# Performance work log

Hardware: AMD Instinct MI355X
Metric: run time of the kernel (lower is better)

## Reference

```python
import jax, jax.numpy as jnp
import numpy as np

B, L, E = 256, 500, 300  # bsz, max_doc_len, word_embed_dim
KS = [3, 5, 7]           # filters_size


def setup_inputs() -> dict:
    key = jax.random.key(0)
    ks = jax.random.split(key, 1 + 2 * len(KS))
    inp = {"x": jax.random.normal(ks[0], (B, L, E), jnp.float32)}
    i = 1
    for k in KS:
        # PyTorch Conv2d default init scale ~ 1/sqrt(fan_in)
        inp[f"aw{k}"] = jax.random.normal(ks[i], (k, E), jnp.float32) / np.sqrt(k * E).astype(np.float32); i += 1
        inp[f"ab{k}"] = jnp.zeros((1,), jnp.float32)
        inp[f"cw{k}"] = jax.random.normal(ks[i], (E,), jnp.float32) / np.sqrt(E).astype(np.float32); i += 1
        inp[f"cb{k}"] = jnpp = jnp.zeros((1,), jnp.float32)
    return inp


def _branch(x, aw, ab, cw, cb):
    # x: (B, L, E); aw: (k, E); cw: (E,)
    k = aw.shape[0]
    p = (k - 1) // 2
    x4 = x[:, None, :, :]            # NCHW: (B, 1, L, E)
    w4 = aw[None, None, :, :]        # OIHW: (1, 1, k, E)
    s = jax.lax.conv_general_dilated(x4, w4, window_strides=(1, 1),
                                     padding=((p, p), (0, 0)))  # (B, 1, L, 1)
    score = jax.nn.sigmoid(s + ab[0])[:, 0, :, :]               # (B, L, 1)
    gated = x * score                                           # broadcast over E
    # Conv2d(1,1,(1,E)) == per-timestep dot product over E
    return jnp.tanh(jnp.einsum('ble,e->bl', gated, cw) + cb[0])  # (B, L)


def reference(x, aw3, ab3, cw3, cb3, aw5, ab5, cw5, cb5, aw7, ab7, cw7, cb7):
    return (_branch(x, aw3, ab3, cw3, cb3),
            _branch(x, aw5, ab5, cw5, cb5),
            _branch(x, aw7, ab7, cw7, cb7))
```

## Files before the change

kernel.cpp:

```cpp
#include <hip/hip_runtime.h>
#include <math.h>

#define BB 256
#define LL 500
#define EE 300
#define NROWS (BB * LL)
#define NJ 18
#define TOUT 56
#define NTILE 9
#define DROWS 64

__global__ __launch_bounds__(256) void fused_kernel(
    const float* __restrict__ x,
    const float* __restrict__ aw3, const float* __restrict__ ab3,
    const float* __restrict__ cw3, const float* __restrict__ cb3,
    const float* __restrict__ aw5, const float* __restrict__ ab5,
    const float* __restrict__ cw5, const float* __restrict__ cb5,
    const float* __restrict__ aw7, const float* __restrict__ ab7,
    const float* __restrict__ cw7, const float* __restrict__ cb7,
    float* __restrict__ out)
{
    __shared__ float dlds[DROWS][NJ + 1];

    const int b    = blockIdx.x / NTILE;
    const int t    = blockIdx.x % NTILE;
    const int l0   = t * TOUT - 3;
    const int wave = threadIdx.x >> 6;
    const int lane = threadIdx.x & 63;
    const int g    = lane >> 4;
    const int j    = lane & 15;
    const int lr   = wave * 16 + g * 4;

    bool valid[4];
    const float4* xr[4];
#pragma unroll
    for (int rr = 0; rr < 4; ++rr) {
        const int l = l0 + lr + rr;
        valid[rr] = (l >= 0) && (l < LL);
        const int lc = l < 0 ? 0 : (l >= LL ? LL - 1 : l);
        xr[rr] = (const float4*)(x + ((size_t)b * LL + lc) * EE);
    }

    const float* const wptr[NJ] = {
        aw3, aw3 + 300, aw3 + 600, cw3,
        aw5, aw5 + 300, aw5 + 600, aw5 + 900, aw5 + 1200, cw5,
        aw7, aw7 + 300, aw7 + 600, aw7 + 900, aw7 + 1200, aw7 + 1500, aw7 + 1800, cw7
    };

    float acc[NJ][4];
#pragma unroll
    for (int d = 0; d < NJ; ++d)
#pragma unroll
        for (int rr = 0; rr < 4; ++rr) acc[d][rr] = 0.0f;

#define BODY(c)                                                                     \
    {                                                                               \
        const float4 x0 = xr[0][(c)];                                               \
        const float4 x1 = xr[1][(c)];                                               \
        const float4 x2 = xr[2][(c)];                                               \
        const float4 x3 = xr[3][(c)];                                               \
        _Pragma("unroll")                                                           \
        for (int d = 0; d < NJ; ++d) {                                              \
            const float4 w = ((const float4*)wptr[d])[(c)];                         \
            acc[d][0] = fmaf(x0.w, w.w, fmaf(x0.z, w.z, fmaf(x0.y, w.y, fmaf(x0.x, w.x, acc[d][0])))); \
            acc[d][1] = fmaf(x1.w, w.w, fmaf(x1.z, w.z, fmaf(x1.y, w.y, fmaf(x1.x, w.x, acc[d][1])))); \
            acc[d][2] = fmaf(x2.w, w.w, fmaf(x2.z, w.z, fmaf(x2.y, w.y, fmaf(x2.x, w.x, acc[d][2])))); \
            acc[d][3] = fmaf(x3.w, w.w, fmaf(x3.z, w.z, fmaf(x3.y, w.y, fmaf(x3.x, w.x, acc[d][3])))); \
        }                                                                           \
    }

    BODY(j)
    BODY(j + 16)
    BODY(j + 32)
    BODY(j + 48)
    if (j < 11) {
        BODY(j + 64)
    }
#undef BODY

#pragma unroll
    for (int d = 0; d < NJ; ++d)
#pragma unroll
        for (int rr = 0; rr < 4; ++rr) {
            float v = acc[d][rr];
            v += __shfl_xor(v, 1, 16);
            v += __shfl_xor(v, 2, 16);
            v += __shfl_xor(v, 4, 16);
            v += __shfl_xor(v, 8, 16);
            acc[d][rr] = v;
        }

#pragma unroll
    for (int rr = 0; rr < 4; ++rr) {
        if (j == rr) {
            const float vf = valid[rr] ? 1.0f : 0.0f;
#pragma unroll
            for (int d = 0; d < NJ; ++d) dlds[lr + rr][d] = acc[d][rr] * vf;
        }
    }

    __syncthreads();

    const int tid = threadIdx.x;
    if (tid < TOUT) {
        const int lo = t * TOUT + tid;
        if (lo < LL) {
            const int c = tid + 3;

            float pre3 = 0.0f, pre5 = 0.0f, pre7 = 0.0f;
#pragma unroll
            for (int tp = 0; tp < 3; ++tp) pre3 += dlds[c + tp - 1][tp];
#pragma unroll
            for (int tp = 0; tp < 5; ++tp) pre5 += dlds[c + tp - 2][4 + tp];
#pragma unroll
            for (int tp = 0; tp < 7; ++tp) pre7 += dlds[c + tp - 3][10 + tp];

            const float c3v = dlds[c][3];
            const float c5v = dlds[c][9];
            const float c7v = dlds[c][17];

            const float s3 = 1.0f / (1.0f + expf(-(pre3 + ab3[0])));
            const float s5 = 1.0f / (1.0f + expf(-(pre5 + ab5[0])));
            const float s7 = 1.0f / (1.0f + expf(-(pre7 + ab7[0])));

            const int r = b * LL + lo;
            out[r]             = tanhf(s3 * c3v + cb3[0]);
            out[NROWS + r]     = tanhf(s5 * c5v + cb5[0]);
            out[2 * NROWS + r] = tanhf(s7 * c7v + cb7[0]);
        }
    }
}

extern "C" void kernel_launch(void* const* d_in, const int* in_sizes, int n_in,
                              void* d_out, int out_size, void* d_ws, size_t ws_size,
                              hipStream_t stream) {
    const float* x   = (const float*)d_in[0];
    const float* aw3 = (const float*)d_in[1];
    const float* ab3 = (const float*)d_in[2];
    const float* cw3 = (const float*)d_in[3];
    const float* cb3 = (const float*)d_in[4];
    const float* aw5 = (const float*)d_in[5];
    const float* ab5 = (const float*)d_in[6];
    const float* cw5 = (const float*)d_in[7];
    const float* cb5 = (const float*)d_in[8];
    const float* aw7 = (const float*)d_in[9];
    const float* ab7 = (const float*)d_in[10];
    const float* cw7 = (const float*)d_in[11];
    const float* cb7 = (const float*)d_in[12];

    float* out = (float*)d_out;

    fused_kernel<<<BB * NTILE, 256, 0, stream>>>(
        x, aw3, ab3, cw3, cb3, aw5, ab5, cw5, cb5, aw7, ab7, cw7, cb7, out);
}
```

Before: 266.4 us.

## Stage filter weights in LDS and software-prefetch x rows

```diff
diff --git a/kernel.cpp b/kernel.cpp
--- a/kernel.cpp
+++ b/kernel.cpp
@@ -6,11 +6,12 @@
 #define EE 300
 #define NROWS (BB * LL)
 #define NJ 18
+#define NC 75
 #define TOUT 56
 #define NTILE 9
 #define DROWS 64
 
-__global__ __launch_bounds__(256) void fused_kernel(
+__global__ __launch_bounds__(256, 4) void fused_kernel(
     const float* __restrict__ x,
     const float* __restrict__ aw3, const float* __restrict__ ab3,
     const float* __restrict__ cw3, const float* __restrict__ cb3,
@@ -20,13 +21,38 @@
     const float* __restrict__ cw7, const float* __restrict__ cb7,
     float* __restrict__ out)
 {
+    __shared__ float4 wlds[NJ][NC];
     __shared__ float dlds[DROWS][NJ + 1];
+    __shared__ const float4* wbase[NJ];
+
+    const int tid = threadIdx.x;
+
+    if (tid == 0) {
+        wbase[0]  = (const float4*)(aw3);
+        wbase[1]  = (const float4*)(aw3 + 300);
+        wbase[2]  = (const float4*)(aw3 + 600);
+        wbase[3]  = (const float4*)(cw3);
+        wbase[4]  = (const float4*)(aw5);
+        wbase[5]  = (const float4*)(aw5 + 300);
+        wbase[6]  = (const float4*)(aw5 + 600);
+        wbase[7]  = (const float4*)(aw5 + 900);
+        wbase[8]  = (const float4*)(aw5 + 1200);
+        wbase[9]  = (const float4*)(cw5);
+        wbase[10] = (const float4*)(aw7);
+        wbase[11] = (const float4*)(aw7 + 300);
+        wbase[12] = (const float4*)(aw7 + 600);
+        wbase[13] = (const float4*)(aw7 + 900);
+        wbase[14] = (const float4*)(aw7 + 1200);
+        wbase[15] = (const float4*)(aw7 + 1500);
+        wbase[16] = (const float4*)(aw7 + 1800);
+        wbase[17] = (const float4*)(cw7);
+    }
 
     const int b    = blockIdx.x / NTILE;
     const int t    = blockIdx.x % NTILE;
     const int l0   = t * TOUT - 3;
-    const int wave = threadIdx.x >> 6;
-    const int lane = threadIdx.x & 63;
+    const int wave = tid >> 6;
+    const int lane = tid & 63;
     const int g    = lane >> 4;
     const int j    = lane & 15;
     const int lr   = wave * 16 + g * 4;
@@ -41,11 +67,17 @@
         xr[rr] = (const float4*)(x + ((size_t)b * LL + lc) * EE);
     }
 
-    const float* const wptr[NJ] = {
-        aw3, aw3 + 300, aw3 + 600, cw3,
-        aw5, aw5 + 300, aw5 + 600, aw5 + 900, aw5 + 1200, cw5,
-        aw7, aw7 + 300, aw7 + 600, aw7 + 900, aw7 + 1200, aw7 + 1500, aw7 + 1800, cw7
-    };
+    float4 xc[4];
+#pragma unroll
+    for (int rr = 0; rr < 4; ++rr) xc[rr] = xr[rr][j];
+
+    __syncthreads();
+    for (int i = tid; i < NJ * NC; i += 256) {
+        const int d = i / NC;
+        const int c = i - d * NC;
+        wlds[d][c] = wbase[d][c];
+    }
+    __syncthreads();
 
     float acc[NJ][4];
 #pragma unroll
@@ -53,30 +85,32 @@
 #pragma unroll
         for (int rr = 0; rr < 4; ++rr) acc[d][rr] = 0.0f;
 
-#define BODY(c)                                                                     \
+#define COMPUTE(c)                                                                  \
     {                                                                               \
-        const float4 x0 = xr[0][(c)];                                               \
-        const float4 x1 = xr[1][(c)];                                               \
-        const float4 x2 = xr[2][(c)];                                               \
-        const float4 x3 = xr[3][(c)];                                               \
         _Pragma("unroll")                                                           \
         for (int d = 0; d < NJ; ++d) {                                              \
-            const float4 w = ((const float4*)wptr[d])[(c)];                         \
-            acc[d][0] = fmaf(x0.w, w.w, fmaf(x0.z, w.z, fmaf(x0.y, w.y, fmaf(x0.x, w.x, acc[d][0])))); \
-            acc[d][1] = fmaf(x1.w, w.w, fmaf(x1.z, w.z, fmaf(x1.y, w.y, fmaf(x1.x, w.x, acc[d][1])))); \
-            acc[d][2] = fmaf(x2.w, w.w, fmaf(x2.z, w.z, fmaf(x2.y, w.y, fmaf(x2.x, w.x, acc[d][2])))); \
-            acc[d][3] = fmaf(x3.w, w.w, fmaf(x3.z, w.z, fmaf(x3.y, w.y, fmaf(x3.x, w.x, acc[d][3])))); \
+            const float4 w = wlds[d][(c)];                                          \
+            acc[d][0] = fmaf(xc[0].w, w.w, fmaf(xc[0].z, w.z, fmaf(xc[0].y, w.y, fmaf(xc[0].x, w.x, acc[d][0])))); \
+            acc[d][1] = fmaf(xc[1].w, w.w, fmaf(xc[1].z, w.z, fmaf(xc[1].y, w.y, fmaf(xc[1].x, w.x, acc[d][1])))); \
+            acc[d][2] = fmaf(xc[2].w, w.w, fmaf(xc[2].z, w.z, fmaf(xc[2].y, w.y, fmaf(xc[2].x, w.x, acc[d][2])))); \
+            acc[d][3] = fmaf(xc[3].w, w.w, fmaf(xc[3].z, w.z, fmaf(xc[3].y, w.y, fmaf(xc[3].x, w.x, acc[d][3])))); \
         }                                                                           \
     }
 
-    BODY(j)
-    BODY(j + 16)
-    BODY(j + 32)
-    BODY(j + 48)
+    float4 xn[4];
+#pragma unroll
+    for (int k = 0; k < 4; ++k) {
+        const int cn = (k == 3) ? ((j < 11) ? (j + 64) : 74) : (j + 16 * (k + 1));
+#pragma unroll
+        for (int rr = 0; rr < 4; ++rr) xn[rr] = xr[rr][cn];
+        COMPUTE(j + 16 * k)
+#pragma unroll
+        for (int rr = 0; rr < 4; ++rr) xc[rr] = xn[rr];
+    }
     if (j < 11) {
-        BODY(j + 64)
+        COMPUTE(j + 64)
     }
-#undef BODY
+#undef COMPUTE
 
 #pragma unroll
     for (int d = 0; d < NJ; ++d)
@@ -101,7 +135,6 @@
 
     __syncthreads();
 
-    const int tid = threadIdx.x;
     if (tid < TOUT) {
         const int lo = t * TOUT + tid;
         if (lo < LL) {
```

Measured after the change: 331.9 us. +24.6%, slower.
